# Kernel tuning notes

Measured on AMD Instinct MI355X. Metric: run time of the kernel, lower is better.

The kernel has to match this reference:

```python
import jax, jax.numpy as jnp
import numpy as np

M_MARGIN = 0.5
SCALE = 64.0
COS_M = float(np.cos(M_MARGIN))
SIN_M = float(np.sin(M_MARGIN))
TH = -COS_M
MM = SIN_M * M_MARGIN
NUM_CLASSES = 100000
IN_FEATURES = 512
BATCH = 512


def setup_inputs() -> dict:
    key = jax.random.key(0)
    k1, k2, k3 = jax.random.split(key, 3)
    x = jax.random.normal(k1, (BATCH, IN_FEATURES), dtype=jnp.float32)
    y = jax.random.randint(k2, (BATCH,), 0, NUM_CLASSES, dtype=jnp.int64 if jax.config.jax_enable_x64 else jnp.int32)
    # xavier_uniform-like init for weight [num_classes, in_features]
    limit = float(np.sqrt(6.0 / (NUM_CLASSES + IN_FEATURES)))
    weight = jax.random.uniform(k3, (NUM_CLASSES, IN_FEATURES), minval=-limit, maxval=limit, dtype=jnp.float32)
    return {"x": x, "y": y, "weight": weight}


def _l2_normalize(v, axis=-1, eps=1e-12):
    # matches F.normalize(p=2): v / max(||v||, eps)
    n = jnp.sqrt(jnp.sum(v * v, axis=axis, keepdims=True))
    return v / jnp.maximum(n, eps)


def reference(x, y, weight):
    # cosine logits: [B, C]
    xn = _l2_normalize(x)
    wn = _l2_normalize(weight)
    cos = jnp.einsum('bd,cd->bc', xn, wn)
    sin = jnp.sqrt(jnp.clip(1.0 - cos * cos, 0.0))
    cos_w_margin = cos * COS_M - sin * SIN_M
    cos_w_margin = jnp.where(cos > TH, cos_w_margin, cos - MM)
    ohe = jax.nn.one_hot(y, NUM_CLASSES, dtype=jnp.bool_)
    logit = jnp.where(ohe, cos_w_margin, cos) * SCALE
    # cross entropy, mean reduction
    logp = jax.nn.log_softmax(logit, axis=-1)
    nll = -jnp.take_along_axis(logp, y[:, None], axis=-1)[:, 0]
    return jnp.mean(nll)
```

## Files before the change

### kernel.cpp

```cpp
#include <hip/hip_runtime.h>
#include <hip/hip_bf16.h>
#include <cstdint>
#include <cstddef>

#define C_CLS   100000
#define D_FEAT  512
#define B_ROWS  512

#define COSM 0.8775825618903728f
#define SINM 0.479425538604203f
#define TH_  (-0.8775825618903728f)
#define MM_  0.2397127693021015f

typedef __bf16 bf16x8 __attribute__((ext_vector_type(8)));
typedef __bf16 bf16x4 __attribute__((ext_vector_type(4)));
typedef float  f32x4  __attribute__((ext_vector_type(4)));

typedef __attribute__((address_space(3))) void lds_void;
typedef const __attribute__((address_space(1))) void g_void;

__device__ __forceinline__ void async_copy16(const void* g, void* l) {
    __builtin_amdgcn_global_load_lds((g_void*)g, (lds_void*)l, 16, 0, 0);
}

__global__ void k_xnorm(const float* __restrict__ x, __bf16* __restrict__ xn,
                        float* __restrict__ row_sum, float* __restrict__ tlogit) {
    const int row  = blockIdx.x;
    const int lane = threadIdx.x;
    const f32x4* p = (const f32x4*)(x + (size_t)row * D_FEAT);
    f32x4 a = p[lane];
    f32x4 b = p[lane + 64];
    float s = a[0]*a[0] + a[1]*a[1] + a[2]*a[2] + a[3]*a[3]
            + b[0]*b[0] + b[1]*b[1] + b[2]*b[2] + b[3]*b[3];
    #pragma unroll
    for (int m = 32; m >= 1; m >>= 1) s += __shfl_xor(s, m, 64);
    const float inv = 1.0f / fmaxf(sqrtf(s), 1e-12f);
    bf16x4 o0 = { (__bf16)(a[0]*inv), (__bf16)(a[1]*inv), (__bf16)(a[2]*inv), (__bf16)(a[3]*inv) };
    bf16x4 o1 = { (__bf16)(b[0]*inv), (__bf16)(b[1]*inv), (__bf16)(b[2]*inv), (__bf16)(b[3]*inv) };
    *(bf16x4*)(xn + (size_t)row * D_FEAT + lane * 4)       = o0;
    *(bf16x4*)(xn + (size_t)row * D_FEAT + 256 + lane * 4) = o1;
    if (lane == 0) { row_sum[row] = 0.0f; tlogit[row] = 0.0f; }
}

__global__ void k_wnorm(const float* __restrict__ w, __bf16* __restrict__ wn) {
    const int row  = blockIdx.x * 4 + (threadIdx.x >> 6);
    const int lane = threadIdx.x & 63;
    if (row >= C_CLS) return;
    const f32x4* p = (const f32x4*)(w + (size_t)row * D_FEAT);
    f32x4 a = p[lane];
    f32x4 b = p[lane + 64];
    float s = a[0]*a[0] + a[1]*a[1] + a[2]*a[2] + a[3]*a[3]
            + b[0]*b[0] + b[1]*b[1] + b[2]*b[2] + b[3]*b[3];
    #pragma unroll
    for (int m = 32; m >= 1; m >>= 1) s += __shfl_xor(s, m, 64);
    const float inv = 1.0f / fmaxf(sqrtf(s), 1e-12f);
    bf16x4 o0 = { (__bf16)(a[0]*inv), (__bf16)(a[1]*inv), (__bf16)(a[2]*inv), (__bf16)(a[3]*inv) };
    bf16x4 o1 = { (__bf16)(b[0]*inv), (__bf16)(b[1]*inv), (__bf16)(b[2]*inv), (__bf16)(b[3]*inv) };
    *(bf16x4*)(wn + (size_t)row * D_FEAT + lane * 4)       = o0;
    *(bf16x4*)(wn + (size_t)row * D_FEAT + 256 + lane * 4) = o1;
}

__global__ __launch_bounds__(256, 2) void k_gemm(
        const __bf16* __restrict__ xn, const __bf16* __restrict__ wn,
        const int* __restrict__ y,
        float* __restrict__ row_sum, float* __restrict__ tlogit) {

    __shared__ __align__(16) __bf16 As[4 * 128 * 8];
    __shared__ __align__(16) __bf16 Bs[4 * 128 * 8];
    __shared__ int ys[128];

    const int tid = threadIdx.x;
    const int bm  = blockIdx.x & 3;
    const int bn  = blockIdx.x >> 2;

    if (tid < 128) ys[tid] = y[bm * 128 + tid];

    const int wave = tid >> 6;
    const int lane = tid & 63;
    const int wm   = wave >> 1;
    const int wn_  = wave & 1;
    const int quad = lane >> 4;
    const int l15  = lane & 15;

    f32x4 acc[4][4];
    #pragma unroll
    for (int i = 0; i < 4; ++i)
        #pragma unroll
        for (int j = 0; j < 4; ++j) acc[i][j] = (f32x4){0.f, 0.f, 0.f, 0.f};

    for (int kt = 0; kt < 16; ++kt) {
        const int k0 = kt * 32;
        #pragma unroll
        for (int i = 0; i < 2; ++i) {
            const int c  = tid + i * 256;
            const int qc = c >> 7, rc = c & 127;
            const __bf16* ga = xn + (size_t)(bm * 128 + rc) * D_FEAT + k0 + qc * 8;
            async_copy16(ga, &As[(size_t)c * 8]);
        }
        #pragma unroll
        for (int i = 0; i < 2; ++i) {
            const int c  = tid + i * 256;
            const int qc = c >> 7, rc = c & 127;
            int grow = bn * 128 + rc; if (grow > C_CLS - 1) grow = C_CLS - 1;
            const __bf16* gb = wn + (size_t)grow * D_FEAT + k0 + qc * 8;
            async_copy16(gb, &Bs[(size_t)c * 8]);
        }
        __syncthreads();

        bf16x8 af[4], bfr[4];
        #pragma unroll
        for (int mi = 0; mi < 4; ++mi) {
            const int r = wm * 64 + mi * 16 + l15;
            af[mi] = *(const bf16x8*)&As[(size_t)(quad * 128 + r) * 8];
        }
        #pragma unroll
        for (int ni = 0; ni < 4; ++ni) {
            const int r = wn_ * 64 + ni * 16 + l15;
            bfr[ni] = *(const bf16x8*)&Bs[(size_t)(quad * 128 + r) * 8];
        }
        #pragma unroll
        for (int mi = 0; mi < 4; ++mi)
            #pragma unroll
            for (int ni = 0; ni < 4; ++ni)
                acc[mi][ni] = __builtin_amdgcn_mfma_f32_16x16x32_bf16(af[mi], bfr[ni], acc[mi][ni], 0, 0, 0);
        __syncthreads();
    }

    #pragma unroll
    for (int mi = 0; mi < 4; ++mi) {
        float rs[4] = {0.f, 0.f, 0.f, 0.f};
        #pragma unroll
        for (int ni = 0; ni < 4; ++ni) {
            const int lcol = wn_ * 64 + ni * 16 + l15;
            const int gcol = bn * 128 + lcol;
            const bool colv = (gcol < C_CLS);
            #pragma unroll
            for (int reg = 0; reg < 4; ++reg) {
                const int lrow = wm * 64 + mi * 16 + quad * 4 + reg;
                const float cosv = acc[mi][ni][reg];
                const float sinv = sqrtf(fmaxf(1.0f - cosv * cosv, 0.0f));
                const float phi  = (cosv > TH_) ? (cosv * COSM - sinv * SINM) : (cosv - MM_);
                const bool ist   = colv && (gcol == ys[lrow]);
                const float logit = 64.0f * (ist ? phi : cosv);
                if (ist) tlogit[bm * 128 + lrow] = logit;
                rs[reg] += colv ? __expf(logit - 64.0f) : 0.0f;
            }
        }
        #pragma unroll
        for (int reg = 0; reg < 4; ++reg) {
            float v = rs[reg];
            v += __shfl_xor(v, 8, 64);
            v += __shfl_xor(v, 4, 64);
            v += __shfl_xor(v, 2, 64);
            v += __shfl_xor(v, 1, 64);
            if (l15 == 0) {
                const int lrow = wm * 64 + mi * 16 + quad * 4 + reg;
                atomicAdd(&row_sum[bm * 128 + lrow], v);
            }
        }
    }
}

__global__ void k_final(const float* __restrict__ row_sum, const float* __restrict__ tlogit,
                        float* __restrict__ out) {
    const int t = threadIdx.x;
    float v = logf(row_sum[t]) + 64.0f - tlogit[t];
    #pragma unroll
    for (int m = 32; m >= 1; m >>= 1) v += __shfl_xor(v, m, 64);
    __shared__ float partial[8];
    if ((t & 63) == 0) partial[t >> 6] = v;
    __syncthreads();
    if (t == 0) {
        float s = 0.f;
        #pragma unroll
        for (int i = 0; i < 8; ++i) s += partial[i];
        out[0] = s * (1.0f / 512.0f);
    }
}

extern "C" void kernel_launch(void* const* d_in, const int* in_sizes, int n_in,
                              void* d_out, int out_size, void* d_ws, size_t ws_size,
                              hipStream_t stream) {
    const float* x = (const float*)d_in[0];
    const int*   y = (const int*)d_in[1];
    const float* w = (const float*)d_in[2];

    char* ws = (char*)d_ws;
    __bf16* xn      = (__bf16*)ws;
    __bf16* wnorm   = (__bf16*)(ws + 524288);
    float*  row_sum = (float*)(ws + 524288 + 102400000);
    float*  tlogit  = (float*)(ws + 524288 + 102400000 + 2048);
    float*  out     = (float*)d_out;

    hipLaunchKernelGGL(k_xnorm, dim3(512), dim3(64), 0, stream, x, xn, row_sum, tlogit);
    hipLaunchKernelGGL(k_wnorm, dim3(25000), dim3(256), 0, stream, w, wnorm);
    hipLaunchKernelGGL(k_gemm, dim3(4 * 782), dim3(256), 0, stream, xn, wnorm, y, row_sum, tlogit);
    hipLaunchKernelGGL(k_final, dim3(1), dim3(512), 0, stream, row_sum, tlogit, out);
}
```

Measured before the change: 509.7 us.

## Load GEMM fragments directly from global into registers with double buffering

The GEMM kernel no longer stages A and B tiles through LDS with async global-to-LDS copies and barriers. Each lane now loads its MFMA fragments straight from global memory, with a register double buffer that prefetches the next k-slice while the current one is multiplied. This removes the per-iteration barriers and LDS traffic, but each tile element is now fetched by both waves that share it, so global and L2 traffic rises. Register pressure also grows under the 2-blocks-per-CU launch bound.

```diff
diff --git a/kernel.cpp b/kernel.cpp
--- a/kernel.cpp
+++ b/kernel.cpp
@@ -15,13 +15,6 @@
 typedef __bf16 bf16x8 __attribute__((ext_vector_type(8)));
 typedef __bf16 bf16x4 __attribute__((ext_vector_type(4)));
 typedef float  f32x4  __attribute__((ext_vector_type(4)));
-
-typedef __attribute__((address_space(3))) void lds_void;
-typedef const __attribute__((address_space(1))) void g_void;
-
-__device__ __forceinline__ void async_copy16(const void* g, void* l) {
-    __builtin_amdgcn_global_load_lds((g_void*)g, (lds_void*)l, 16, 0, 0);
-}
 
 __global__ void k_xnorm(const float* __restrict__ x, __bf16* __restrict__ xn,
                         float* __restrict__ row_sum, float* __restrict__ tlogit) {
@@ -65,8 +58,6 @@
         const int* __restrict__ y,
         float* __restrict__ row_sum, float* __restrict__ tlogit) {
 
-    __shared__ __align__(16) __bf16 As[4 * 128 * 8];
-    __shared__ __align__(16) __bf16 Bs[4 * 128 * 8];
     __shared__ int ys[128];
 
     const int tid = threadIdx.x;
@@ -82,49 +73,49 @@
     const int quad = lane >> 4;
     const int l15  = lane & 15;
 
+    const __bf16* ap[4];
+    const __bf16* bp[4];
+    #pragma unroll
+    for (int i = 0; i < 4; ++i) {
+        const int ar = bm * 128 + wm * 64 + i * 16 + l15;
+        ap[i] = xn + (size_t)ar * D_FEAT + quad * 8;
+        int br = bn * 128 + wn_ * 64 + i * 16 + l15;
+        if (br > C_CLS - 1) br = C_CLS - 1;
+        bp[i] = wn + (size_t)br * D_FEAT + quad * 8;
+    }
+
     f32x4 acc[4][4];
     #pragma unroll
     for (int i = 0; i < 4; ++i)
         #pragma unroll
         for (int j = 0; j < 4; ++j) acc[i][j] = (f32x4){0.f, 0.f, 0.f, 0.f};
 
+    bf16x8 a[2][4], b[2][4];
+    #pragma unroll
+    for (int i = 0; i < 4; ++i) {
+        a[0][i] = *(const bf16x8*)(ap[i]);
+        b[0][i] = *(const bf16x8*)(bp[i]);
+    }
+
+    #pragma unroll
     for (int kt = 0; kt < 16; ++kt) {
-        const int k0 = kt * 32;
-        #pragma unroll
-        for (int i = 0; i < 2; ++i) {
-            const int c  = tid + i * 256;
-            const int qc = c >> 7, rc = c & 127;
-            const __bf16* ga = xn + (size_t)(bm * 128 + rc) * D_FEAT + k0 + qc * 8;
-            async_copy16(ga, &As[(size_t)c * 8]);
-        }
-        #pragma unroll
-        for (int i = 0; i < 2; ++i) {
-            const int c  = tid + i * 256;
-            const int qc = c >> 7, rc = c & 127;
-            int grow = bn * 128 + rc; if (grow > C_CLS - 1) grow = C_CLS - 1;
-            const __bf16* gb = wn + (size_t)grow * D_FEAT + k0 + qc * 8;
-            async_copy16(gb, &Bs[(size_t)c * 8]);
-        }
-        __syncthreads();
-
-        bf16x8 af[4], bfr[4];
-        #pragma unroll
-        for (int mi = 0; mi < 4; ++mi) {
-            const int r = wm * 64 + mi * 16 + l15;
-            af[mi] = *(const bf16x8*)&As[(size_t)(quad * 128 + r) * 8];
-        }
-        #pragma unroll
-        for (int ni = 0; ni < 4; ++ni) {
-            const int r = wn_ * 64 + ni * 16 + l15;
-            bfr[ni] = *(const bf16x8*)&Bs[(size_t)(quad * 128 + r) * 8];
+        const int cur = kt & 1, nxt = cur ^ 1;
+        if (kt < 15) {
+            const int ko = (kt + 1) * 32;
+            #pragma unroll
+            for (int i = 0; i < 4; ++i) {
+                a[nxt][i] = *(const bf16x8*)(ap[i] + ko);
+                b[nxt][i] = *(const bf16x8*)(bp[i] + ko);
+            }
         }
         #pragma unroll
         for (int mi = 0; mi < 4; ++mi)
             #pragma unroll
             for (int ni = 0; ni < 4; ++ni)
-                acc[mi][ni] = __builtin_amdgcn_mfma_f32_16x16x32_bf16(af[mi], bfr[ni], acc[mi][ni], 0, 0, 0);
-        __syncthreads();
+                acc[mi][ni] = __builtin_amdgcn_mfma_f32_16x16x32_bf16(a[cur][mi], b[cur][ni], acc[mi][ni], 0, 0, 0);
     }
+
+    __syncthreads();
 
     #pragma unroll
     for (int mi = 0; mi < 4; ++mi) {
```

Measured after the change: 679.1 us. 33.2% more time.

## Use row-major LDS tiles for coalesced loads and precompute global addresses

Applied to the files above, without the earlier changes.

Changes the LDS tile layout from k-chunk-major to row-major, with 32 bf16 per row, so each four consecutive threads fetch one contiguous 64-byte row segment. This replaces strided global accesses with coalesced ones. Per-thread global pointers are now computed once outside the k loop, and launch bounds are raised to 3 blocks per CU. The risk is that the row-major layout, with a 64-byte row stride, may cause LDS bank conflicts on the fragment reads, and the tighter register budget may cause spills.

```diff
diff --git a/kernel.cpp b/kernel.cpp
--- a/kernel.cpp
+++ b/kernel.cpp
@@ -60,13 +60,13 @@
     *(bf16x4*)(wn + (size_t)row * D_FEAT + 256 + lane * 4) = o1;
 }
 
-__global__ __launch_bounds__(256, 2) void k_gemm(
+__global__ __launch_bounds__(256, 3) void k_gemm(
         const __bf16* __restrict__ xn, const __bf16* __restrict__ wn,
         const int* __restrict__ y,
         float* __restrict__ row_sum, float* __restrict__ tlogit) {
 
-    __shared__ __align__(16) __bf16 As[4 * 128 * 8];
-    __shared__ __align__(16) __bf16 Bs[4 * 128 * 8];
+    __shared__ __align__(16) __bf16 As[128 * 32];
+    __shared__ __align__(16) __bf16 Bs[128 * 32];
     __shared__ int ys[128];
 
     const int tid = threadIdx.x;
@@ -82,6 +82,16 @@
     const int quad = lane >> 4;
     const int l15  = lane & 15;
 
+    const int c0 = tid, c1 = tid + 256;
+    const int r0 = c0 >> 2, kc0 = (c0 & 3) * 8;
+    const int r1 = c1 >> 2, kc1 = (c1 & 3) * 8;
+    int bw0 = bn * 128 + r0; if (bw0 > C_CLS - 1) bw0 = C_CLS - 1;
+    int bw1 = bn * 128 + r1; if (bw1 > C_CLS - 1) bw1 = C_CLS - 1;
+    const __bf16* ga0 = xn + (size_t)(bm * 128 + r0) * D_FEAT + kc0;
+    const __bf16* ga1 = xn + (size_t)(bm * 128 + r1) * D_FEAT + kc1;
+    const __bf16* gb0 = wn + (size_t)bw0 * D_FEAT + kc0;
+    const __bf16* gb1 = wn + (size_t)bw1 * D_FEAT + kc1;
+
     f32x4 acc[4][4];
     #pragma unroll
     for (int i = 0; i < 4; ++i)
@@ -90,33 +100,22 @@
 
     for (int kt = 0; kt < 16; ++kt) {
         const int k0 = kt * 32;
-        #pragma unroll
-        for (int i = 0; i < 2; ++i) {
-            const int c  = tid + i * 256;
-            const int qc = c >> 7, rc = c & 127;
-            const __bf16* ga = xn + (size_t)(bm * 128 + rc) * D_FEAT + k0 + qc * 8;
-            async_copy16(ga, &As[(size_t)c * 8]);
-        }
-        #pragma unroll
-        for (int i = 0; i < 2; ++i) {
-            const int c  = tid + i * 256;
-            const int qc = c >> 7, rc = c & 127;
-            int grow = bn * 128 + rc; if (grow > C_CLS - 1) grow = C_CLS - 1;
-            const __bf16* gb = wn + (size_t)grow * D_FEAT + k0 + qc * 8;
-            async_copy16(gb, &Bs[(size_t)c * 8]);
-        }
+        async_copy16(ga0 + k0, &As[(size_t)c0 * 8]);
+        async_copy16(ga1 + k0, &As[(size_t)c1 * 8]);
+        async_copy16(gb0 + k0, &Bs[(size_t)c0 * 8]);
+        async_copy16(gb1 + k0, &Bs[(size_t)c1 * 8]);
         __syncthreads();
 
         bf16x8 af[4], bfr[4];
         #pragma unroll
         for (int mi = 0; mi < 4; ++mi) {
             const int r = wm * 64 + mi * 16 + l15;
-            af[mi] = *(const bf16x8*)&As[(size_t)(quad * 128 + r) * 8];
+            af[mi] = *(const bf16x8*)&As[(size_t)r * 32 + quad * 8];
         }
         #pragma unroll
         for (int ni = 0; ni < 4; ++ni) {
             const int r = wn_ * 64 + ni * 16 + l15;
-            bfr[ni] = *(const bf16x8*)&Bs[(size_t)(quad * 128 + r) * 8];
+            bfr[ni] = *(const bf16x8*)&Bs[(size_t)r * 32 + quad * 8];
         }
         #pragma unroll
         for (int mi = 0; mi < 4; ++mi)
```

Result: slower. 527.3 us (+3.5%).
